# Optimization experiments

Measured on AMD Instinct MI355X. Metric: run time of the kernel, lower is better.

The kernel has to match this reference:

```python
import jax, jax.numpy as jnp
import numpy as np

H = 16  # num_attention_heads

def setup_inputs() -> dict:
    key = jax.random.key(0)
    ks = jax.random.split(key, 4)
    B, S, D = 4, 2048, 1024
    scale = 1.0 / np.sqrt(D)
    return {
        "hidden_states": jax.random.normal(ks[0], (B, S, D), dtype=jnp.float32),
        "attention_mask": jnp.zeros((B, 1, 1, S), dtype=jnp.float32),
        "Wq": jax.random.normal(ks[1], (D, D), dtype=jnp.float32) * scale,
        "bq": jnp.zeros((D,), dtype=jnp.float32),
        "Wk": jax.random.normal(ks[2], (D, D), dtype=jnp.float32) * scale,
        "bk": jnp.zeros((D,), dtype=jnp.float32),
        "Wv": jax.random.normal(ks[3], (D, D), dtype=jnp.float32) * scale,
        "bv": jnp.zeros((D,), dtype=jnp.float32),
    }

def _split_heads(x, B, S):
    # [B,S,D] -> [B,H,S,Dh]
    return x.reshape(B, S, H, -1).transpose(0, 2, 1, 3)

def reference(hidden_states, attention_mask, Wq, bq, Wk, bk, Wv, bv):
    B, S, D = hidden_states.shape
    Dh = D // H
    q = _split_heads(hidden_states @ Wq.T + bq, B, S)  # [B,H,S,Dh]
    k = _split_heads(hidden_states @ Wk.T + bk, B, S)
    v = _split_heads(hidden_states @ Wv.T + bv, B, S)
    scores = jnp.einsum("bhqd,bhkd->bhqk", q, k) / jnp.sqrt(jnp.float32(Dh))
    scores = scores + attention_mask  # additive mask, broadcast [B,1,1,S]
    probs = jax.nn.softmax(scores, axis=-1)  # dropout is identity in eval mode
    ctx = jnp.einsum("bhqk,bhkd->bhqd", probs, v)  # [B,H,S,Dh]
    ctx = ctx.transpose(0, 2, 1, 3).reshape(B, S, D)
    return ctx
```

## Files before the change

### kernel.cpp

```cpp
#include <hip/hip_runtime.h>
#include <hip/hip_bf16.h>
#include <stdint.h>

#define LOG2E 1.44269504088896340736f
#define SCL   (0.125f * LOG2E)

typedef __attribute__((ext_vector_type(8)))  short short8;
typedef __attribute__((ext_vector_type(16))) float floatx16;
typedef __attribute__((ext_vector_type(4)))  unsigned short ushort4v;

#define GLP(g, l)                                                              \
    __builtin_amdgcn_global_load_lds(                                          \
        (const __attribute__((address_space(1))) void*)(g),                    \
        (__attribute__((address_space(3))) void*)(l), 16, 0, 0)

#if __has_builtin(__builtin_amdgcn_exp2f)
#define EXP2(x) __builtin_amdgcn_exp2f(x)
#else
#define EXP2(x) exp2f(x)
#endif

static __device__ __forceinline__ unsigned short f2bf(float f) {
    union { float f; unsigned u; } v; v.f = f;
    unsigned r = v.u + 0x7FFFu + ((v.u >> 16) & 1u);
    return (unsigned short)(r >> 16);
}

static __device__ __forceinline__ unsigned pack2bf(float a, float b) {
    __hip_bfloat162 h = __float22bfloat162_rn(make_float2(a, b));
    union { __hip_bfloat162 h; unsigned u; } c; c.h = h; return c.u;
}

__global__ __launch_bounds__(256) void cvt_all(const float* __restrict__ X,
                                               const float* __restrict__ Wq,
                                               const float* __restrict__ Wk,
                                               const float* __restrict__ Wv,
                                               const float* __restrict__ mask,
                                               unsigned short* __restrict__ xb,
                                               unsigned short* __restrict__ wb,
                                               float* __restrict__ maskl) {
    int i = blockIdx.x * 256 + threadIdx.x;
    if (i < 2097152) {
        float4 v = ((const float4*)X)[i];
        ushort4v o;
        o.x = f2bf(v.x); o.y = f2bf(v.y); o.z = f2bf(v.z); o.w = f2bf(v.w);
        ((ushort4v*)xb)[i] = o;
    } else if (i < 2883584) {
        int j = i - 2097152;
        const float* src; int k;
        if (j < 262144)      { src = Wq; k = j; }
        else if (j < 524288) { src = Wk; k = j - 262144; }
        else                 { src = Wv; k = j - 524288; }
        float4 v = ((const float4*)src)[k];
        ushort4v o;
        o.x = f2bf(v.x); o.y = f2bf(v.y); o.z = f2bf(v.z); o.w = f2bf(v.w);
        ((ushort4v*)wb)[j] = o;
    } else if (i < 2883584 + 2048) {
        int j = i - 2883584;
        float4 v = ((const float4*)mask)[j];
        ((float4*)maskl)[j] = make_float4(v.x * LOG2E, v.y * LOG2E,
                                          v.z * LOG2E, v.w * LOG2E);
    }
}

__global__ __launch_bounds__(256) void qkv_gemm(
        const unsigned short* __restrict__ X,
        const unsigned short* __restrict__ W,
        const float* __restrict__ bq, const float* __restrict__ bk,
        const float* __restrict__ bv,
        unsigned short* __restrict__ Qf,
        unsigned short* __restrict__ Kf,
        unsigned short* __restrict__ Vt)
{
    __shared__ __align__(16) unsigned short sh[17408];
    unsigned short* Ash = sh;
    unsigned short* Bsh = sh + 8192;

    const int tid  = threadIdx.x;
    const int lane = tid & 63;
    const int wv   = tid >> 6;
    const int q32  = lane & 31;
    const int hi   = lane >> 5;
    const int mBase = blockIdx.x * 128;
    const int nBase = blockIdx.y * 128;
    const int wm = (wv >> 1) * 64;
    const int wn = (wv & 1) * 64;

    floatx16 acc[2][2];
    acc[0][0] = 0.0f; acc[0][1] = 0.0f; acc[1][0] = 0.0f; acc[1][1] = 0.0f;

    const int sr = lane >> 3;
    const int kc = (lane & 7) ^ sr;

    for (int kb = 0; kb < 1024; kb += 64) {
        __syncthreads();
#pragma unroll
        for (int s = 0; s < 4; ++s) {
            const int seg = wv * 4 + s;
            const int row = seg * 8 + sr;
            GLP(X + (size_t)(mBase + row) * 1024 + kb + kc * 8, Ash + seg * 512);
            GLP(W + (size_t)(nBase + row) * 1024 + kb + kc * 8, Bsh + seg * 512);
        }
        __syncthreads();
#pragma unroll
        for (int ks = 0; ks < 4; ++ks) {
            short8 aF[2], bF[2];
#pragma unroll
            for (int mi = 0; mi < 2; ++mi) {
                const int R = wm + mi * 32 + q32;
                const int slot = (2 * ks + hi) ^ (R & 7);
                aF[mi] = *(const short8*)(Ash + (R >> 3) * 512 + (R & 7) * 64 + slot * 8);
            }
#pragma unroll
            for (int ni = 0; ni < 2; ++ni) {
                const int R = wn + ni * 32 + q32;
                const int slot = (2 * ks + hi) ^ (R & 7);
                bF[ni] = *(const short8*)(Bsh + (R >> 3) * 512 + (R & 7) * 64 + slot * 8);
            }
#pragma unroll
            for (int mi = 0; mi < 2; ++mi)
#pragma unroll
                for (int ni = 0; ni < 2; ++ni)
                    acc[mi][ni] = __builtin_amdgcn_mfma_f32_32x32x16_bf16(
                        aF[mi], bF[ni], acc[mi][ni], 0, 0, 0);
        }
    }

    if (blockIdx.y < 16) {
        unsigned short* dst = (blockIdx.y < 8) ? Qf : Kf;
        const float* bias   = (blockIdx.y < 8) ? bq : bk;
        const float scl     = (blockIdx.y < 8) ? SCL : 1.0f;
        const int nb = nBase & 1023;
        float bj[2];
#pragma unroll
        for (int ni = 0; ni < 2; ++ni)
            bj[ni] = bias[nb + wn + ni * 32 + q32];
        __syncthreads();
#pragma unroll
        for (int ni = 0; ni < 2; ++ni) {
            const int col = wn + ni * 32 + q32;
#pragma unroll
            for (int mi = 0; mi < 2; ++mi)
#pragma unroll
                for (int g = 0; g < 4; ++g) {
                    const int row0 = wm + mi * 32 + g * 8 + hi * 4;
#pragma unroll
                    for (int rr = 0; rr < 4; ++rr)
                        sh[(row0 + rr) * 136 + col] =
                            f2bf((acc[mi][ni][g * 4 + rr] + bj[ni]) * scl);
                }
        }
        __syncthreads();
#pragma unroll
        for (int it = 0; it < 8; ++it) {
            const int row  = it * 16 + (tid >> 4);
            const int part = tid & 15;
            short8 v = *(const short8*)(sh + row * 136 + part * 8);
            *(short8*)(dst + (size_t)(mBase + row) * 1024 + nb + part * 8) = v;
        }
    } else {
#pragma unroll
        for (int ni = 0; ni < 2; ++ni) {
            const int gn = nBase + wn + ni * 32 + q32;
            const int c  = gn & 1023;
            const int h  = c >> 6;
            const int d  = c & 63;
            const float bias = bv[c];
#pragma unroll
            for (int mi = 0; mi < 2; ++mi)
#pragma unroll
                for (int g = 0; g < 4; ++g) {
                    const int m0 = mBase + wm + mi * 32 + g * 8 + hi * 4;
                    const int b  = m0 >> 11;
                    const int s0 = m0 & 2047;
                    const int sp = (s0 & ~12) | ((s0 & 4) << 1) | ((s0 & 8) >> 1);
                    ushort4v pv;
#pragma unroll
                    for (int rr = 0; rr < 4; ++rr)
                        pv[rr] = f2bf(acc[mi][ni][g * 4 + rr] + bias);
                    *(ushort4v*)(Vt + (size_t)((b * 16 + h) * 64 + d) * 2048 + sp) = pv;
                }
        }
    }
}

__global__ __launch_bounds__(256, 2) void attn_kernel(
        const unsigned short* __restrict__ Qf,
        const unsigned short* __restrict__ Kf,
        const unsigned short* __restrict__ VT,
        const float* __restrict__ maskl,
        float* __restrict__ out)
{
    __shared__ __align__(16) unsigned short Ksh[2 * 128 * 64];
    __shared__ __align__(16) unsigned short Vsh[2 * 64 * 128];
    __shared__ __align__(16) float Msh[2 * 132];
    __shared__ __align__(16) float Lsh[128];

    const int tid  = threadIdx.x;
    const int lane = tid & 63;
    const int wv   = tid >> 6;
    const int q32  = lane & 31;
    const int hi   = lane >> 5;
    const int bh   = blockIdx.x & 63;
    const int qt   = blockIdx.x >> 6;
    const int b    = bh >> 4;
    const int h    = bh & 15;
    const int q0   = qt * 128 + wv * 32;
    const int sw   = q32 & 7;

    short8 bQ[4];
#pragma unroll
    for (int ks = 0; ks < 4; ++ks)
        bQ[ks] = *(const short8*)(Qf + (size_t)(b * 2048 + q0 + q32) * 1024
                                     + h * 64 + ks * 16 + hi * 8);

    floatx16 accO0 = 0.0f, accO1 = 0.0f;
    float l_c = 0.0f;

    const unsigned short* gK = Kf + (size_t)(b * 2048) * 1024 + h * 64;
    const unsigned short* gV = VT + (size_t)(bh * 64) * 2048;
    const float* mrow = maskl + b * 2048;

    const unsigned short* kb4[4];
    const unsigned short* vb4[4];
#pragma unroll
    for (int ks = 0; ks < 4; ++ks) {
        const int cs = (2 * ks + hi) ^ sw;
        kb4[ks] = Ksh + q32 * 64 + cs * 8;
        vb4[ks] = Vsh + q32 * 128 + cs * 8;
    }

    const int krr = lane >> 3;
    const int kcs = lane & 7;
    const int vrr = lane >> 4;
    const int vcs = lane & 15;

    auto STAGE = [&](int kbn, int so, int mo) {
#pragma unroll
        for (int s = 0; s < 4; ++s) {
            const int seg = wv * 4 + s;
            const int rK  = seg * 8 + krr;
            const int cK  = kcs ^ (rK & 7);
            GLP(gK + (size_t)(kbn + rK) * 1024 + cK * 8, Ksh + so + seg * 512);
            const int rV  = seg * 4 + vrr;
            const int cV  = vcs ^ (rV & 7);
            GLP(gV + (size_t)rV * 2048 + kbn + cV * 8, Vsh + so + seg * 512);
        }
        if (tid < 32) GLP(mrow + kbn + lane * 4, Msh + mo);
    };

    auto TILE = [&](int kb, int ro, int mo, int so, int smo) {
        if (kb + 128 < 2048) STAGE(kb + 128, so, smo);
        const float* mb = Msh + mo + hi * 4;
#pragma unroll
        for (int half = 0; half < 2; ++half) {
#pragma unroll
            for (int mt = 0; mt < 2; ++mt) {
                floatx16 sacc;
#pragma unroll
                for (int a = 0; a < 4; ++a) {
                    float4 mv4 = *(const float4*)(mb + half * 64 + mt * 32 + a * 8);
                    sacc[a * 4 + 0] = mv4.x; sacc[a * 4 + 1] = mv4.y;
                    sacc[a * 4 + 2] = mv4.z; sacc[a * 4 + 3] = mv4.w;
                }
                __builtin_amdgcn_s_setprio(1);
#pragma unroll
                for (int ks = 0; ks < 4; ++ks) {
                    short8 aK = *(const short8*)(kb4[ks] + ro + half * 4096 + mt * 2048);
                    sacc = __builtin_amdgcn_mfma_f32_32x32x16_bf16(aK, bQ[ks], sacc, 0, 0, 0);
                }
                __builtin_amdgcn_s_setprio(0);
                unsigned u[8];
#pragma unroll
                for (int a = 0; a < 4; ++a) {
                    float p0 = EXP2(sacc[a * 4 + 0]);
                    float p1 = EXP2(sacc[a * 4 + 1]);
                    float p2 = EXP2(sacc[a * 4 + 2]);
                    float p3 = EXP2(sacc[a * 4 + 3]);
                    l_c += (p0 + p1) + (p2 + p3);
                    u[2 * a]     = pack2bf(p0, p1);
                    u[2 * a + 1] = pack2bf(p2, p3);
                }
#pragma unroll
                for (int ks2 = 0; ks2 < 2; ++ks2) {
                    union { unsigned uu[4]; short8 s; } aP;
                    aP.uu[0] = u[4 * ks2 + 0];
                    aP.uu[1] = u[4 * ks2 + 1];
                    aP.uu[2] = u[4 * ks2 + 2];
                    aP.uu[3] = u[4 * ks2 + 3];
                    const int ks = mt * 2 + ks2;
                    short8 bV0 = *(const short8*)(vb4[ks] + ro + half * 64);
                    short8 bV1 = *(const short8*)(vb4[ks] + ro + 4096 + half * 64);
                    __builtin_amdgcn_s_setprio(1);
                    accO0 = __builtin_amdgcn_mfma_f32_32x32x16_bf16(aP.s, bV0, accO0, 0, 0, 0);
                    accO1 = __builtin_amdgcn_mfma_f32_32x32x16_bf16(aP.s, bV1, accO1, 0, 0, 0);
                    __builtin_amdgcn_s_setprio(0);
                }
            }
        }
        asm volatile("s_waitcnt vmcnt(0) lgkmcnt(0)" ::: "memory");
        __builtin_amdgcn_s_barrier();
    };

    STAGE(0, 0, 0);
    asm volatile("s_waitcnt vmcnt(0)" ::: "memory");
    __builtin_amdgcn_s_barrier();

#pragma unroll 1
    for (int kb2 = 0; kb2 < 2048; kb2 += 256) {
        TILE(kb2,       0,    0,   8192, 132);
        TILE(kb2 + 128, 8192, 132, 0,    0);
    }

    l_c += __shfl_xor(l_c, 32, 64);
    if (lane < 32) Lsh[wv * 32 + q32] = 1.0f / l_c;
#pragma unroll
    for (int g = 0; g < 4; ++g) {
        float4 inv4 = *(const float4*)(Lsh + wv * 32 + g * 8 + hi * 4);
#pragma unroll
        for (int rr = 0; rr < 4; ++rr) {
            const int r   = g * 4 + rr;
            const int row = rr + 8 * g + 4 * hi;
            const float linv = (rr == 0) ? inv4.x : (rr == 1) ? inv4.y
                             : (rr == 2) ? inv4.z : inv4.w;
            float* op = out + (size_t)(b * 2048 + q0 + row) * 1024 + h * 64 + q32;
            op[0]  = accO0[r] * linv;
            op[32] = accO1[r] * linv;
        }
    }
}

extern "C" void kernel_launch(void* const* d_in, const int* in_sizes, int n_in,
                              void* d_out, int out_size, void* d_ws, size_t ws_size,
                              hipStream_t stream) {
    const float* X    = (const float*)d_in[0];
    const float* mask = (const float*)d_in[1];
    const float* Wq   = (const float*)d_in[2];
    const float* bq   = (const float*)d_in[3];
    const float* Wk   = (const float*)d_in[4];
    const float* bk   = (const float*)d_in[5];
    const float* Wv   = (const float*)d_in[6];
    const float* bv   = (const float*)d_in[7];
    float* out = (float*)d_out;

    char* ws = (char*)d_ws;
    unsigned short* xb  = (unsigned short*)(ws);
    unsigned short* wb  = (unsigned short*)(ws + 16777216);
    unsigned short* qf  = (unsigned short*)(ws + 23068672);
    unsigned short* kf  = (unsigned short*)(ws + 39845888);
    unsigned short* vtb = (unsigned short*)(ws + 56623104);
    float*          ml  = (float*)(ws + 73400320);

    cvt_all<<<11272, 256, 0, stream>>>(X, Wq, Wk, Wv, mask, xb, wb, ml);

    qkv_gemm<<<dim3(64, 24), 256, 0, stream>>>(xb, wb, bq, bk, bv, qf, kf, vtb);

    attn_kernel<<<1024, 256, 0, stream>>>(qf, kf, vtb, ml, out);
}
```

Measured before the change: 246.7 us.

## Double per-wave query rows in attention, compute row sums via MFMA

Each wave now handles 64 query rows instead of 32, so every K/V tile loaded into LDS is reused across twice as many queries, and the grid is halved to 512 blocks. Softmax row sums are accumulated by multiplying P with a ones vector on the matrix cores rather than with scalar adds plus a shuffle and an LDS exchange. The mask for the whole row is loaded into LDS once at the start rather than staged per tile. Register pressure roughly doubles for the accumulators, and occupancy is pinned through waves_per_eu, so spills or fewer resident blocks are possible; 512 blocks may also underfill the GPU.

Result: no change. 242.0 us (-1.9%).

```diff
diff --git a/kernel.cpp b/kernel.cpp
--- a/kernel.cpp
+++ b/kernel.cpp
@@ -30,6 +30,15 @@
     __hip_bfloat162 h = __float22bfloat162_rn(make_float2(a, b));
     union { __hip_bfloat162 h; unsigned u; } c; c.h = h; return c.u;
 }
+
+#define EXPPACK(dst, sv, base) do {                                            \
+        float p0 = EXP2((sv)[(base) + 0]), p1 = EXP2((sv)[(base) + 1]);        \
+        float p2 = EXP2((sv)[(base) + 2]), p3 = EXP2((sv)[(base) + 3]);        \
+        float p4 = EXP2((sv)[(base) + 4]), p5 = EXP2((sv)[(base) + 5]);        \
+        float p6 = EXP2((sv)[(base) + 6]), p7 = EXP2((sv)[(base) + 7]);        \
+        dst.uu[0] = pack2bf(p0, p1); dst.uu[1] = pack2bf(p2, p3);              \
+        dst.uu[2] = pack2bf(p4, p5); dst.uu[3] = pack2bf(p6, p7);              \
+    } while (0)
 
 __global__ __launch_bounds__(256) void cvt_all(const float* __restrict__ X,
                                                const float* __restrict__ Wq,
@@ -184,7 +193,8 @@
     }
 }
 
-__global__ __launch_bounds__(256, 2) void attn_kernel(
+__global__ __launch_bounds__(256)
+__attribute__((amdgpu_waves_per_eu(2, 2))) void attn_kernel(
         const unsigned short* __restrict__ Qf,
         const unsigned short* __restrict__ Kf,
         const unsigned short* __restrict__ VT,
@@ -193,8 +203,7 @@
 {
     __shared__ __align__(16) unsigned short Ksh[2 * 128 * 64];
     __shared__ __align__(16) unsigned short Vsh[2 * 64 * 128];
-    __shared__ __align__(16) float Msh[2 * 132];
-    __shared__ __align__(16) float Lsh[128];
+    __shared__ __align__(16) float Mall[2048];
 
     const int tid  = threadIdx.x;
     const int lane = tid & 63;
@@ -205,17 +214,25 @@
     const int qt   = blockIdx.x >> 6;
     const int b    = bh >> 4;
     const int h    = bh & 15;
-    const int q0   = qt * 128 + wv * 32;
+    const int q0   = qt * 256 + wv * 64;
     const int sw   = q32 & 7;
 
-    short8 bQ[4];
-#pragma unroll
-    for (int ks = 0; ks < 4; ++ks)
-        bQ[ks] = *(const short8*)(Qf + (size_t)(b * 2048 + q0 + q32) * 1024
-                                     + h * 64 + ks * 16 + hi * 8);
-
-    floatx16 accO0 = 0.0f, accO1 = 0.0f;
-    float l_c = 0.0f;
+    short8 bQ0[4], bQ1[4];
+#pragma unroll
+    for (int ks = 0; ks < 4; ++ks) {
+        bQ0[ks] = *(const short8*)(Qf + (size_t)(b * 2048 + q0 + q32) * 1024
+                                      + h * 64 + ks * 16 + hi * 8);
+        bQ1[ks] = *(const short8*)(Qf + (size_t)(b * 2048 + q0 + 32 + q32) * 1024
+                                      + h * 64 + ks * 16 + hi * 8);
+    }
+
+    short8 ones;
+#pragma unroll
+    for (int j = 0; j < 8; ++j) ones[j] = (short)0x3F80;
+
+    floatx16 accO00 = 0.0f, accO01 = 0.0f;
+    floatx16 accO10 = 0.0f, accO11 = 0.0f;
+    floatx16 lacc0 = 0.0f, lacc1 = 0.0f;
 
     const unsigned short* gK = Kf + (size_t)(b * 2048) * 1024 + h * 64;
     const unsigned short* gV = VT + (size_t)(bh * 64) * 2048;
@@ -235,7 +252,7 @@
     const int vrr = lane >> 4;
     const int vcs = lane & 15;
 
-    auto STAGE = [&](int kbn, int so, int mo) {
+    auto STAGE = [&](int kbn, int so) {
 #pragma unroll
         for (int s = 0; s < 4; ++s) {
             const int seg = wv * 4 + s;
@@ -246,88 +263,96 @@
             const int cV  = vcs ^ (rV & 7);
             GLP(gV + (size_t)rV * 2048 + kbn + cV * 8, Vsh + so + seg * 512);
         }
-        if (tid < 32) GLP(mrow + kbn + lane * 4, Msh + mo);
     };
 
-    auto TILE = [&](int kb, int ro, int mo, int so, int smo) {
-        if (kb + 128 < 2048) STAGE(kb + 128, so, smo);
-        const float* mb = Msh + mo + hi * 4;
-#pragma unroll
+    auto TILE = [&](int kb, int ro, int so) {
+        if (kb + 128 < 2048) STAGE(kb + 128, so);
+        const float* mloc = Mall + kb + hi * 4;
+#pragma unroll 1
         for (int half = 0; half < 2; ++half) {
+            short8 aK0[4], aK1[4];
+#pragma unroll
+            for (int ks = 0; ks < 4; ++ks) {
+                aK0[ks] = *(const short8*)(kb4[ks] + ro + half * 4096);
+                aK1[ks] = *(const short8*)(kb4[ks] + ro + half * 4096 + 2048);
+            }
+            const float* mh = mloc + half * 64;
 #pragma unroll
             for (int mt = 0; mt < 2; ++mt) {
-                floatx16 sacc;
+                const short8* aK = (mt == 0) ? aK0 : aK1;
+                floatx16 mC;
 #pragma unroll
                 for (int a = 0; a < 4; ++a) {
-                    float4 mv4 = *(const float4*)(mb + half * 64 + mt * 32 + a * 8);
-                    sacc[a * 4 + 0] = mv4.x; sacc[a * 4 + 1] = mv4.y;
-                    sacc[a * 4 + 2] = mv4.z; sacc[a * 4 + 3] = mv4.w;
+                    float4 mv = *(const float4*)(mh + mt * 32 + a * 8);
+                    mC[4 * a + 0] = mv.x; mC[4 * a + 1] = mv.y;
+                    mC[4 * a + 2] = mv.z; mC[4 * a + 3] = mv.w;
                 }
                 __builtin_amdgcn_s_setprio(1);
-#pragma unroll
-                for (int ks = 0; ks < 4; ++ks) {
-                    short8 aK = *(const short8*)(kb4[ks] + ro + half * 4096 + mt * 2048);
-                    sacc = __builtin_amdgcn_mfma_f32_32x32x16_bf16(aK, bQ[ks], sacc, 0, 0, 0);
+                floatx16 s0 = __builtin_amdgcn_mfma_f32_32x32x16_bf16(aK[0], bQ0[0], mC, 0, 0, 0);
+                floatx16 s1 = __builtin_amdgcn_mfma_f32_32x32x16_bf16(aK[0], bQ1[0], mC, 0, 0, 0);
+#pragma unroll
+                for (int ks = 1; ks < 4; ++ks) {
+                    s0 = __builtin_amdgcn_mfma_f32_32x32x16_bf16(aK[ks], bQ0[ks], s0, 0, 0, 0);
+                    s1 = __builtin_amdgcn_mfma_f32_32x32x16_bf16(aK[ks], bQ1[ks], s1, 0, 0, 0);
                 }
                 __builtin_amdgcn_s_setprio(0);
-                unsigned u[8];
-#pragma unroll
-                for (int a = 0; a < 4; ++a) {
-                    float p0 = EXP2(sacc[a * 4 + 0]);
-                    float p1 = EXP2(sacc[a * 4 + 1]);
-                    float p2 = EXP2(sacc[a * 4 + 2]);
-                    float p3 = EXP2(sacc[a * 4 + 3]);
-                    l_c += (p0 + p1) + (p2 + p3);
-                    u[2 * a]     = pack2bf(p0, p1);
-                    u[2 * a + 1] = pack2bf(p2, p3);
-                }
-#pragma unroll
-                for (int ks2 = 0; ks2 < 2; ++ks2) {
-                    union { unsigned uu[4]; short8 s; } aP;
-                    aP.uu[0] = u[4 * ks2 + 0];
-                    aP.uu[1] = u[4 * ks2 + 1];
-                    aP.uu[2] = u[4 * ks2 + 2];
-                    aP.uu[3] = u[4 * ks2 + 3];
-                    const int ks = mt * 2 + ks2;
-                    short8 bV0 = *(const short8*)(vb4[ks] + ro + half * 64);
-                    short8 bV1 = *(const short8*)(vb4[ks] + ro + 4096 + half * 64);
-                    __builtin_amdgcn_s_setprio(1);
-                    accO0 = __builtin_amdgcn_mfma_f32_32x32x16_bf16(aP.s, bV0, accO0, 0, 0, 0);
-                    accO1 = __builtin_amdgcn_mfma_f32_32x32x16_bf16(aP.s, bV1, accO1, 0, 0, 0);
-                    __builtin_amdgcn_s_setprio(0);
-                }
+                short8 bVa0 = *(const short8*)(vb4[2 * mt + 0] + ro + half * 64);
+                short8 bVa1 = *(const short8*)(vb4[2 * mt + 0] + ro + 4096 + half * 64);
+                short8 bVb0 = *(const short8*)(vb4[2 * mt + 1] + ro + half * 64);
+                short8 bVb1 = *(const short8*)(vb4[2 * mt + 1] + ro + 4096 + half * 64);
+                union { unsigned uu[4]; short8 s; } aPa, aPb, aPc, aPd;
+                EXPPACK(aPa, s0, 0);
+                EXPPACK(aPb, s0, 8);
+                EXPPACK(aPc, s1, 0);
+                EXPPACK(aPd, s1, 8);
+                __builtin_amdgcn_s_setprio(1);
+                accO00 = __builtin_amdgcn_mfma_f32_32x32x16_bf16(aPa.s, bVa0, accO00, 0, 0, 0);
+                accO01 = __builtin_amdgcn_mfma_f32_32x32x16_bf16(aPa.s, bVa1, accO01, 0, 0, 0);
+                lacc0  = __builtin_amdgcn_mfma_f32_32x32x16_bf16(aPa.s, ones, lacc0, 0, 0, 0);
+                accO00 = __builtin_amdgcn_mfma_f32_32x32x16_bf16(aPb.s, bVb0, accO00, 0, 0, 0);
+                accO01 = __builtin_amdgcn_mfma_f32_32x32x16_bf16(aPb.s, bVb1, accO01, 0, 0, 0);
+                lacc0  = __builtin_amdgcn_mfma_f32_32x32x16_bf16(aPb.s, ones, lacc0, 0, 0, 0);
+                accO10 = __builtin_amdgcn_mfma_f32_32x32x16_bf16(aPc.s, bVa0, accO10, 0, 0, 0);
+                accO11 = __builtin_amdgcn_mfma_f32_32x32x16_bf16(aPc.s, bVa1, accO11, 0, 0, 0);
+                lacc1  = __builtin_amdgcn_mfma_f32_32x32x16_bf16(aPc.s, ones, lacc1, 0, 0, 0);
+                accO10 = __builtin_amdgcn_mfma_f32_32x32x16_bf16(aPd.s, bVb0, accO10, 0, 0, 0);
+                accO11 = __builtin_amdgcn_mfma_f32_32x32x16_bf16(aPd.s, bVb1, accO11, 0, 0, 0);
+                lacc1  = __builtin_amdgcn_mfma_f32_32x32x16_bf16(aPd.s, ones, lacc1, 0, 0, 0);
+                __builtin_amdgcn_s_setprio(0);
             }
         }
         asm volatile("s_waitcnt vmcnt(0) lgkmcnt(0)" ::: "memory");
         __builtin_amdgcn_s_barrier();
     };
 
-    STAGE(0, 0, 0);
+#pragma unroll
+    for (int s = 0; s < 2; ++s)
+        GLP(mrow + (wv * 2 + s) * 256 + lane * 4, Mall + (wv * 2 + s) * 256);
+    STAGE(0, 0);
     asm volatile("s_waitcnt vmcnt(0)" ::: "memory");
     __builtin_amdgcn_s_barrier();
 
 #pragma unroll 1
     for (int kb2 = 0; kb2 < 2048; kb2 += 256) {
-        TILE(kb2,       0,    0,   8192, 132);
-        TILE(kb2 + 128, 8192, 132, 0,    0);
-    }
-
-    l_c += __shfl_xor(l_c, 32, 64);
-    if (lane < 32) Lsh[wv * 32 + q32] = 1.0f / l_c;
-#pragma unroll
-    for (int g = 0; g < 4; ++g) {
-        float4 inv4 = *(const float4*)(Lsh + wv * 32 + g * 8 + hi * 4);
+        TILE(kb2,       0,    8192);
+        TILE(kb2 + 128, 8192, 0);
+    }
+
+#pragma unroll
+    for (int g = 0; g < 4; ++g)
 #pragma unroll
         for (int rr = 0; rr < 4; ++rr) {
             const int r   = g * 4 + rr;
             const int row = rr + 8 * g + 4 * hi;
-            const float linv = (rr == 0) ? inv4.x : (rr == 1) ? inv4.y
-                             : (rr == 2) ? inv4.z : inv4.w;
-            float* op = out + (size_t)(b * 2048 + q0 + row) * 1024 + h * 64 + q32;
-            op[0]  = accO0[r] * linv;
-            op[32] = accO1[r] * linv;
-        }
-    }
+            const float li0 = 1.0f / lacc0[r];
+            const float li1 = 1.0f / lacc1[r];
+            float* op0 = out + (size_t)(b * 2048 + q0 + row) * 1024 + h * 64 + q32;
+            float* op1 = out + (size_t)(b * 2048 + q0 + 32 + row) * 1024 + h * 64 + q32;
+            op0[0]  = accO00[r] * li0;
+            op0[32] = accO01[r] * li0;
+            op1[0]  = accO10[r] * li1;
+            op1[32] = accO11[r] * li1;
+        }
 }
 
 extern "C" void kernel_launch(void* const* d_in, const int* in_sizes, int n_in,
@@ -355,5 +380,5 @@
 
     qkv_gemm<<<dim3(64, 24), 256, 0, stream>>>(xb, wb, bq, bk, bv, qf, kf, vtb);
 
-    attn_kernel<<<1024, 256, 0, stream>>>(qf, kf, vtb, ml, out);
-}
+    attn_kernel<<<512, 256, 0, stream>>>(qf, kf, vtb, ml, out);
+}
```
